# Optimization experiments

Measured on AMD Instinct MI355X. Metric: run time of the kernel, lower is better.

## Reference

```python
import jax, jax.numpy as jnp
import numpy as np

T, B, E, H, F = 1024, 2, 1024, 16, 8
D = E // H
R = 2 * T - 1  # relative positions T-1 .. -(T-1)


def setup_inputs() -> dict:
    key = jax.random.key(0)
    ks = jax.random.split(key, 11)
    std = float(np.sqrt(2.0 / (E + E)))
    return {
        "input": jax.random.normal(ks[0], (T, B, E), jnp.float32),
        "pos": jax.random.normal(ks[1], (R, B, E), jnp.float32),
        "factor": jax.random.normal(ks[2], (F,), jnp.float32),
        "in_proj_weight": jax.random.normal(ks[3], (3 * E * E, F), jnp.float32) * std,
        "pos_proj_weight": jax.random.normal(ks[4], (E * E, F), jnp.float32) * std,
        "out_proj_weight": jax.random.normal(ks[5], (E * E, F), jnp.float32) * std,
        "in_proj_bias": jax.random.normal(ks[6], (3 * E, F), jnp.float32) * 0.02,
        "pos_proj_bias": jax.random.normal(ks[7], (E, F), jnp.float32) * 0.02,
        "out_proj_bias": jax.random.normal(ks[8], (E, F), jnp.float32) * 0.02,
        "r_w_bias": jax.random.normal(ks[9], (E, F), jnp.float32) * 0.02,
        "r_r_bias": jax.random.normal(ks[10], (E, F), jnp.float32) * 0.02,
    }


def _rel_shift(x):
    # x: [BH, T, R] -> out[b, i, j] = x[b, i, j + (T-1) - i]
    bh, q, r = x.shape
    zp = jnp.zeros((bh, q, 1), x.dtype)
    xp = jnp.concatenate([zp, x], axis=2).reshape(bh, r + 1, q)
    return xp[:, 1:, :].reshape(bh, q, r)


def reference(input, pos, factor, in_proj_weight, pos_proj_weight, out_proj_weight,
              in_proj_bias, pos_proj_bias, out_proj_bias, r_w_bias, r_r_bias):
    # hypernetwork: generate effective weights from factor vector (torch.mv)
    W_in = (in_proj_weight @ factor).reshape(3 * E, E)
    W_pos = (pos_proj_weight @ factor).reshape(E, E)
    W_out = (out_proj_weight @ factor).reshape(E, E)
    b_in = in_proj_bias @ factor
    b_pos = pos_proj_bias @ factor
    b_out = out_proj_bias @ factor
    rw = (r_w_bias @ factor).reshape(H, D)  # content bias
    rr = (r_r_bias @ factor).reshape(H, D)  # position bias

    qkv = input @ W_in.T + b_in                      # [T, B, 3E]
    q, k, v = jnp.split(qkv, 3, axis=-1)
    q = q.reshape(T, B, H, D)
    k = k.reshape(T, B, H, D)
    v = v.reshape(T, B, H, D)
    r = (pos @ W_pos.T + b_pos).reshape(R, B, H, D)  # [R, B, H, D]

    scale = 1.0 / np.sqrt(D)
    # AC: content-content + content bias term
    AC = jnp.einsum('ibhd,jbhd->bhij', q + rw, k)    # [B, H, T, T]
    # BD: content-position + position bias term, then relative shift
    BD = jnp.einsum('ibhd,rbhd->bhir', q + rr, r)    # [B, H, T, R]
    BD = _rel_shift(BD.reshape(B * H, T, R))[:, :, :T].reshape(B, H, T, T)

    attn = jax.nn.softmax((AC + BD) * scale, axis=-1)  # [B, H, T, T]
    out = jnp.einsum('bhij,jbhd->ibhd', attn, v).reshape(T, B, E)
    out = out @ W_out.T + b_out                       # [T, B, E]
    return out
```

## Files before the change

### kernel.cpp

```cpp
#include <hip/hip_runtime.h>


typedef _Float16 h16;
typedef _Float16 h16x8 __attribute__((ext_vector_type(8)));
typedef _Float16 h16x4 __attribute__((ext_vector_type(4)));
typedef float f32x4 __attribute__((ext_vector_type(4)));

static __device__ __forceinline__ f32x4 mfma16(h16x8 a, h16x8 b, f32x4 c) {
  return __builtin_amdgcn_mfma_f32_16x16x32_f16(a, b, c, 0, 0, 0);
}
static __device__ __forceinline__ void gload16(const void* g, void* l) {
  __builtin_amdgcn_global_load_lds((const __attribute__((address_space(1))) void*)g,
                                   (__attribute__((address_space(3))) void*)l, 16, 0, 0);
}

__global__ __launch_bounds__(256) void hypernet_kernel(
    const float* __restrict__ fac,
    const float* __restrict__ w_in, const float* __restrict__ w_pos,
    const float* __restrict__ w_out, const float* __restrict__ b_in_w,
    const float* __restrict__ b_pos_w, const float* __restrict__ b_out_w,
    const float* __restrict__ rw_w, const float* __restrict__ rr_w,
    h16* __restrict__ Win, h16* __restrict__ Wpos, h16* __restrict__ Wout,
    float* __restrict__ bin, float* __restrict__ bpos, float* __restrict__ bout,
    float* __restrict__ rw, float* __restrict__ rr, h16* __restrict__ rb,
    const float* __restrict__ input, h16* __restrict__ in_h,
    const float* __restrict__ pos, h16* __restrict__ pos_h)
{
  int idx = blockIdx.x * 256 + threadIdx.x;
  float f0=fac[0],f1=fac[1],f2=fac[2],f3=fac[3],f4=fac[4],f5=fac[5],f6=fac[6],f7=fac[7];
#define DOT8(p) ((p)[0]*f0+(p)[1]*f1+(p)[2]*f2+(p)[3]*f3+(p)[4]*f4+(p)[5]*f5+(p)[6]*f6+(p)[7]*f7)
  if (idx < 3145728) { const float* p = w_in  + (size_t)idx*8; Win[idx]  = (h16)DOT8(p); return; }
  idx -= 3145728;
  if (idx < 1048576) { const float* p = w_pos + (size_t)idx*8; Wpos[idx] = (h16)DOT8(p); return; }
  idx -= 1048576;
  if (idx < 1048576) { const float* p = w_out + (size_t)idx*8; Wout[idx] = (h16)DOT8(p); return; }
  idx -= 1048576;
  if (idx < 3072) { bin[idx]  = DOT8(b_in_w  + (size_t)idx*8); return; }
  idx -= 3072;
  if (idx < 1024) { bpos[idx] = DOT8(b_pos_w + (size_t)idx*8); return; }
  idx -= 1024;
  if (idx < 1024) { bout[idx] = DOT8(b_out_w + (size_t)idx*8); return; }
  idx -= 1024;
  if (idx < 1024) { rw[idx]   = DOT8(rw_w    + (size_t)idx*8); return; }
  idx -= 1024;
  if (idx < 1024) { rr[idx]   = DOT8(rr_w    + (size_t)idx*8); return; }
  idx -= 1024;
  if (idx < 2048) { rb[(((size_t)(idx >> 6)) << 17) + 2047*64 + (idx & 63)] = (h16)0.f; return; }
  idx -= 2048;
  if (idx < 524288) {
    float4 v = reinterpret_cast<const float4*>(input)[idx];
    h16x4 o = { (h16)v.x, (h16)v.y, (h16)v.z, (h16)v.w };
    reinterpret_cast<h16x4*>(in_h)[idx] = o;
    return;
  }
  idx -= 524288;
  if (idx < 1048064) {
    float4 v = reinterpret_cast<const float4*>(pos)[idx];
    h16x4 o = { (h16)v.x, (h16)v.y, (h16)v.z, (h16)v.w };
    reinterpret_cast<h16x4*>(pos_h)[idx] = o;
  }
#undef DOT8
}

template <int MODE>
__global__ __launch_bounds__(256) void gemm_lds_kernel(
    const h16* __restrict__ A, const h16* __restrict__ Bw,
    const float* __restrict__ bias, int M, int N, int K,
    float* __restrict__ Cout,
    const float* __restrict__ rwv, const float* __restrict__ rrv,
    h16* __restrict__ o0, h16* __restrict__ o1,
    h16* __restrict__ o2, h16* __restrict__ o3)
{
  __shared__ __align__(16) h16 a_sm[128*64];
  __shared__ __align__(16) h16 b_sm[128*64];
  const int tid = threadIdx.x, lane = tid & 63, wave = tid >> 6;
  const int quad = lane >> 4, t16 = lane & 15;
  const int wm = wave >> 1, wn = wave & 1;
  const int m0 = blockIdx.y * 128, n0 = blockIdx.x * 128;
  const int lrow = lane >> 3, lgran = lane & 7;
  const int gsw = (lgran ^ lrow) * 8;
  const int xg0 = (quad ^ (t16 & 7)) * 8;
  const int xg1 = xg0 ^ 32;

  f32x4 acc[4][4];
#pragma unroll
  for (int i = 0; i < 4; ++i)
#pragma unroll
    for (int j = 0; j < 4; ++j) acc[i][j] = (f32x4){0.f,0.f,0.f,0.f};

  for (int k0 = 0; k0 < K; k0 += 64) {
    __syncthreads();
#pragma unroll
    for (int s = 0; s < 4; ++s) {
      int rbase = wave*32 + s*8;
      gload16(A  + (size_t)(m0 + rbase + lrow)*K + k0 + gsw, a_sm + rbase*64);
      gload16(Bw + (size_t)(n0 + rbase + lrow)*K + k0 + gsw, b_sm + rbase*64);
    }
    __syncthreads();
#pragma unroll
    for (int kc = 0; kc < 2; ++kc) {
      const int xg = kc ? xg1 : xg0;
      h16x8 af[4], bfr[4];
#pragma unroll
      for (int i = 0; i < 4; ++i) {
        af[i]  = *reinterpret_cast<const h16x8*>(a_sm + (wm*64 + i*16 + t16)*64 + xg);
        bfr[i] = *reinterpret_cast<const h16x8*>(b_sm + (wn*64 + i*16 + t16)*64 + xg);
      }
#pragma unroll
      for (int i = 0; i < 4; ++i)
#pragma unroll
        for (int j = 0; j < 4; ++j)
          acc[i][j] = mfma16(af[i], bfr[j], acc[i][j]);
    }
  }

#pragma unroll
  for (int i = 0; i < 4; ++i) {
    int mb = m0 + wm*64 + i*16 + quad*4;
#pragma unroll
    for (int j = 0; j < 4; ++j) {
      int n = n0 + wn*64 + j*16 + t16;
      float bv = bias[n];
      if (MODE == 2) {
#pragma unroll
        for (int r = 0; r < 4; ++r)
          Cout[(size_t)(mb + r)*N + n] = acc[i][j][r] + bv;
      } else if (MODE == 0) {
        int nn = n & 1023, sec = n >> 10, hh = nn >> 6, d = nn & 63;
        float rwb = rwv[nn], rrb = rrv[nn];
#pragma unroll
        for (int r = 0; r < 4; ++r) {
          int m = mb + r, t = m >> 1, b = m & 1;
          size_t off = ((size_t)((b << 4) + hh) << 16) + (t << 6) + d;
          float v = acc[i][j][r] + bv;
          if (sec == 0)      { o0[off] = (h16)(v + rwb); o1[off] = (h16)(v + rrb); }
          else if (sec == 1) { o2[off] = (h16)v; }
          else               { o3[off] = (h16)v; }
        }
      } else {
        int hh = n >> 6, d = n & 63;
#pragma unroll
        for (int r = 0; r < 4; ++r) {
          int m = mb + r;
          if (m < M) {
            int rel = m >> 1, b = m & 1;
            o0[(((size_t)((b << 4) + hh)) << 17) + (rel << 6) + d] = (h16)(acc[i][j][r] + bv);
          }
        }
      }
    }
  }
}

__global__ __launch_bounds__(256) void transpose_v_kernel(
    const h16* __restrict__ vb, h16* __restrict__ vbt)
{
  __shared__ h16 tile[64*72];
  const int bh = blockIdx.y, t0 = blockIdx.x * 64;
  const int r = threadIdx.x >> 3, c = (threadIdx.x & 7) * 8;
  const h16* src = vb + ((size_t)bh << 16) + (size_t)(t0 + r)*64 + c;
  *reinterpret_cast<h16x8*>(tile + r*72 + c)        = *reinterpret_cast<const h16x8*>(src);
  *reinterpret_cast<h16x8*>(tile + (r + 32)*72 + c) = *reinterpret_cast<const h16x8*>(src + 32*64);
  __syncthreads();
  h16x8 o0, o1;
#pragma unroll
  for (int e = 0; e < 8; ++e) {
    o0[e] = tile[(c + e)*72 + r];
    o1[e] = tile[(c + e)*72 + r + 32];
  }
  h16* dst = vbt + ((size_t)bh << 16) + (size_t)r*1024 + t0 + c;
  *reinterpret_cast<h16x8*>(dst)            = o0;
  *reinterpret_cast<h16x8*>(dst + 32*1024)  = o1;
}

__global__ __launch_bounds__(256) void flash_kernel(
    const h16* __restrict__ qrw, const h16* __restrict__ qrr,
    const h16* __restrict__ kb, const h16* __restrict__ vbt,
    const h16* __restrict__ rb,
    float* __restrict__ o_part, float* __restrict__ ml_part)
{
  __shared__ __align__(16) h16 k_sm[64*64];
  __shared__ __align__(16) h16 vt_sm[64*64];
  __shared__ __align__(16) h16 r_sm[128*64];

  const int tid = threadIdx.x, lane = tid & 63, wave = tid >> 6;
  const int quad = lane >> 4, t16 = lane & 15;
  const int bh = blockIdx.y, i0 = blockIdx.x * 64, jh = blockIdx.z;
  const size_t base  = (size_t)bh << 16;
  const size_t rbase = (size_t)bh << 17;
  const int iw = i0 + wave * 16;
  const int lrow = lane >> 3, lgran = lane & 7;
  const int gsw = (lgran ^ lrow) * 8;
  const int xg0 = (quad ^ (t16 & 7)) * 8;
  const int xg1 = xg0 ^ 32;

  h16x8 a_rw[2], a_rr[2];
  {
    const h16* p = qrw + base + (size_t)(iw + t16)*64 + quad*8;
    a_rw[0] = *reinterpret_cast<const h16x8*>(p);
    a_rw[1] = *reinterpret_cast<const h16x8*>(p + 32);
    const h16* p2 = qrr + base + (size_t)(iw + t16)*64 + quad*8;
    a_rr[0] = *reinterpret_cast<const h16x8*>(p2);
    a_rr[1] = *reinterpret_cast<const h16x8*>(p2 + 32);
  }

  f32x4 o_acc[4];
#pragma unroll
  for (int dc = 0; dc < 4; ++dc) o_acc[dc] = (f32x4){0.f,0.f,0.f,0.f};
  float m_run[4] = {-1e30f,-1e30f,-1e30f,-1e30f};
  float l_run[4] = {0.f,0.f,0.f,0.f};

  h16* bdw = r_sm + wave * (16*84);
  const int cb0 = 3 - wave;

  for (int j0 = jh*256; j0 < jh*256 + 256; j0 += 64) {
    __syncthreads();
    {
#pragma unroll
      for (int s = 0; s < 2; ++s) {
        int row = wave*16 + s*8;
        gload16(kb  + base + (size_t)(j0 + row + lrow)*64 + gsw, k_sm  + row*64);
        gload16(vbt + base + (size_t)(row + lrow)*1024 + j0 + gsw, vt_sm + row*64);
      }
      const int rel0 = j0 - i0 + 960;
#pragma unroll
      for (int s = 0; s < 4; ++s) {
        int row = wave*32 + s*8;
        gload16(rb + rbase + (size_t)(rel0 + row + lrow)*64 + gsw, r_sm + row*64);
      }
    }
    __syncthreads();

    f32x4 s_ac[4];
#pragma unroll
    for (int c = 0; c < 4; ++c) {
      s_ac[c] = (f32x4){0.f,0.f,0.f,0.f};
      s_ac[c] = mfma16(a_rw[0], *reinterpret_cast<const h16x8*>(k_sm + (c*16 + t16)*64 + xg0), s_ac[c]);
      s_ac[c] = mfma16(a_rw[1], *reinterpret_cast<const h16x8*>(k_sm + (c*16 + t16)*64 + xg1), s_ac[c]);
    }
    f32x4 s_bd[5];
#pragma unroll
    for (int u = 0; u < 5; ++u) {
      s_bd[u] = (f32x4){0.f,0.f,0.f,0.f};
      s_bd[u] = mfma16(a_rr[0], *reinterpret_cast<const h16x8*>(r_sm + ((cb0+u)*16 + t16)*64 + xg0), s_bd[u]);
      s_bd[u] = mfma16(a_rr[1], *reinterpret_cast<const h16x8*>(r_sm + ((cb0+u)*16 + t16)*64 + xg1), s_bd[u]);
    }
    __syncthreads();

#pragma unroll
    for (int u = 0; u < 5; ++u)
#pragma unroll
      for (int r = 0; r < 4; ++r)
        bdw[(quad*4 + r)*84 + u*16 + t16] = (h16)s_bd[u][r];

    float sv[4][4];
#pragma unroll
    for (int c = 0; c < 4; ++c)
#pragma unroll
      for (int r = 0; r < 4; ++r) {
        int il = quad*4 + r;
        float bdv = (float)bdw[il*84 + c*16 + t16 + 15 - il];
        sv[c][r] = (s_ac[c][r] + bdv) * 0.125f;
      }

    float alpha[4];
#pragma unroll
    for (int r = 0; r < 4; ++r) {
      float v = fmaxf(fmaxf(sv[0][r], sv[1][r]), fmaxf(sv[2][r], sv[3][r]));
#pragma unroll
      for (int off = 1; off < 16; off <<= 1) v = fmaxf(v, __shfl_xor(v, off, 64));
      float mn = fmaxf(m_run[r], v);
      alpha[r] = __expf(m_run[r] - mn);
      m_run[r] = mn;
    }
#pragma unroll
    for (int r = 0; r < 4; ++r) {
      float s0 = 0.f;
#pragma unroll
      for (int c = 0; c < 4; ++c) {
        float p = __expf(sv[c][r] - m_run[r]);
        sv[c][r] = p; s0 += p;
      }
      l_run[r] = l_run[r]*alpha[r] + s0;
    }
#pragma unroll
    for (int dc = 0; dc < 4; ++dc) {
      f32x4 t = o_acc[dc];
#pragma unroll
      for (int r = 0; r < 4; ++r) t[r] *= alpha[r];
      o_acc[dc] = t;
    }
    h16* pw = bdw;
#pragma unroll
    for (int c = 0; c < 4; ++c)
#pragma unroll
      for (int r = 0; r < 4; ++r)
        pw[(quad*4 + r)*72 + c*16 + t16] = (h16)sv[c][r];

    h16x8 ap0 = *reinterpret_cast<const h16x8*>(pw + t16*72 + quad*8);
    h16x8 ap1 = *reinterpret_cast<const h16x8*>(pw + t16*72 + 32 + quad*8);
#pragma unroll
    for (int dc = 0; dc < 4; ++dc) {
      h16x8 bv0 = *reinterpret_cast<const h16x8*>(vt_sm + (dc*16 + t16)*64 + xg0);
      h16x8 bv1 = *reinterpret_cast<const h16x8*>(vt_sm + (dc*16 + t16)*64 + xg1);
      o_acc[dc] = mfma16(ap0, bv0, o_acc[dc]);
      o_acc[dc] = mfma16(ap1, bv1, o_acc[dc]);
    }
  }

#pragma unroll
  for (int r = 0; r < 4; ++r) {
    float l = l_run[r];
#pragma unroll
    for (int off = 1; off < 16; off <<= 1) l += __shfl_xor(l, off, 64);
    l_run[r] = l;
  }
  const size_t obase = ((size_t)jh*32 + bh) * 1024 * 64;
#pragma unroll
  for (int r = 0; r < 4; ++r) {
    int i = iw + quad*4 + r;
#pragma unroll
    for (int dc = 0; dc < 4; ++dc)
      o_part[obase + (size_t)i*64 + dc*16 + t16] = o_acc[dc][r];
    if (t16 == 0) {
      size_t mo = (((size_t)jh*32 + bh)*1024 + i)*2;
      ml_part[mo]     = m_run[r];
      ml_part[mo + 1] = l_run[r];
    }
  }
}

__global__ __launch_bounds__(256) void combine_kernel(
    const float* __restrict__ o_part, const float* __restrict__ ml_part,
    h16* __restrict__ attn_h)
{
  int gid = blockIdx.x * 256 + threadIdx.x;
  int row = gid >> 4;
  int d4 = (gid & 15) * 4;
  float m[4], l[4];
#pragma unroll
  for (int p = 0; p < 4; ++p) {
    m[p] = ml_part[p*65536 + row*2];
    l[p] = ml_part[p*65536 + row*2 + 1];
  }
  float M = fmaxf(fmaxf(m[0], m[1]), fmaxf(m[2], m[3]));
  float e[4], den = 0.f;
#pragma unroll
  for (int p = 0; p < 4; ++p) { e[p] = __expf(m[p] - M); den += e[p]*l[p]; }
  float inv = 1.f / den;
  float4 acc = {0.f,0.f,0.f,0.f};
#pragma unroll
  for (int p = 0; p < 4; ++p) {
    float4 O = *reinterpret_cast<const float4*>(o_part + (size_t)p*2097152 + (size_t)row*64 + d4);
    acc.x += e[p]*O.x; acc.y += e[p]*O.y; acc.z += e[p]*O.z; acc.w += e[p]*O.w;
  }
  int bh = row >> 10, i = row & 1023, b = bh >> 4, h = bh & 15;
  h16x4 o = { (h16)(acc.x*inv), (h16)(acc.y*inv), (h16)(acc.z*inv), (h16)(acc.w*inv) };
  *reinterpret_cast<h16x4*>(attn_h + ((size_t)(i*2 + b))*1024 + h*64 + d4) = o;
}

extern "C" void kernel_launch(void* const* d_in, const int* in_sizes, int n_in,
                              void* d_out, int out_size, void* d_ws, size_t ws_size,
                              hipStream_t stream)
{
  const float* input  = (const float*)d_in[0];
  const float* pos    = (const float*)d_in[1];
  const float* fac    = (const float*)d_in[2];
  const float* w_in   = (const float*)d_in[3];
  const float* w_pos  = (const float*)d_in[4];
  const float* w_out  = (const float*)d_in[5];
  const float* bin_w  = (const float*)d_in[6];
  const float* bpos_w = (const float*)d_in[7];
  const float* bout_w = (const float*)d_in[8];
  const float* rw_w   = (const float*)d_in[9];
  const float* rr_w   = (const float*)d_in[10];
  float* out = (float*)d_out;
  (void)in_sizes; (void)n_in; (void)out_size; (void)ws_size;

  char* w = (char*)d_ws;
  auto take = [&](size_t bytes) { char* p = w; w += bytes; return p; };
  h16*   Win    = (h16*)take(3145728ull*2);
  h16*   Wpos   = (h16*)take(1048576ull*2);
  h16*   Wout   = (h16*)take(1048576ull*2);
  float* bin    = (float*)take(3072*4);
  float* bpos   = (float*)take(1024*4);
  float* bout   = (float*)take(1024*4);
  float* rw     = (float*)take(1024*4);
  float* rr     = (float*)take(1024*4);
  h16*   in_h   = (h16*)take(2097152ull*2);
  h16*   pos_h  = (h16*)take(4192256ull*2);
  h16*   qrwb   = (h16*)take(2097152ull*2);
  h16*   qrrb   = (h16*)take(2097152ull*2);
  h16*   kb     = (h16*)take(2097152ull*2);
  h16*   vb     = (h16*)take(2097152ull*2);
  h16*   vbt    = (h16*)take(2097152ull*2);
  h16*   rb     = (h16*)take(4194304ull*2);
  float* o_part = (float*)take(4ull*2097152ull*4);
  float* ml     = (float*)take(4ull*65536ull*4);
  h16*   attn_h = (h16*)take(2097152ull*2);

  hypernet_kernel<<<26658, 256, 0, stream>>>(fac, w_in, w_pos, w_out, bin_w, bpos_w, bout_w,
                                             rw_w, rr_w, Win, Wpos, Wout, bin, bpos, bout,
                                             rw, rr, rb, input, in_h, pos, pos_h);
  gemm_lds_kernel<0><<<dim3(24, 16), 256, 0, stream>>>(in_h, Win, bin, 2048, 3072, 1024,
                                                       nullptr, rw, rr, qrwb, qrrb, kb, vb);
  gemm_lds_kernel<1><<<dim3(8, 32), 256, 0, stream>>>(pos_h, Wpos, bpos, 4094, 1024, 1024,
                                                      nullptr, nullptr, nullptr, rb, nullptr, nullptr, nullptr);
  transpose_v_kernel<<<dim3(16, 32), 256, 0, stream>>>(vb, vbt);
  flash_kernel<<<dim3(16, 32, 4), 256, 0, stream>>>(qrwb, qrrb, kb, vbt, rb, o_part, ml);
  combine_kernel<<<2048, 256, 0, stream>>>(o_part, ml, attn_h);
  gemm_lds_kernel<2><<<dim3(8, 16), 256, 0, stream>>>(attn_h, Wout, bout, 2048, 1024, 1024,
                                                      out, nullptr, nullptr, nullptr, nullptr, nullptr, nullptr);
}
```

Measured before the change: 356.7 us.

## Vectorize hypernet weight generation and fuse V transpose into QKV GEMM epilogue

The hypernetwork kernel now handles eight outputs per thread. It uses float4 loads of each 8-wide factor row and writes into the contiguous Win/Wpos/Wout and in_h/pos_h workspace regions as single flat arrays, which cuts the grid size and per-thread branching. The separate V transpose kernel and its intermediate buffer are removed. The QKV GEMM epilogue now writes V directly in transposed [d, t] layout. This saves a launch and a round trip through memory, but the new scattered 2-byte epilogue stores have a 1024-element stride and are poorly coalesced.

```diff
diff --git a/kernel.cpp b/kernel.cpp
--- a/kernel.cpp
+++ b/kernel.cpp
@@ -20,46 +20,83 @@
     const float* __restrict__ w_out, const float* __restrict__ b_in_w,
     const float* __restrict__ b_pos_w, const float* __restrict__ b_out_w,
     const float* __restrict__ rw_w, const float* __restrict__ rr_w,
-    h16* __restrict__ Win, h16* __restrict__ Wpos, h16* __restrict__ Wout,
+    h16* __restrict__ Wall,
     float* __restrict__ bin, float* __restrict__ bpos, float* __restrict__ bout,
     float* __restrict__ rw, float* __restrict__ rr, h16* __restrict__ rb,
-    const float* __restrict__ input, h16* __restrict__ in_h,
-    const float* __restrict__ pos, h16* __restrict__ pos_h)
+    const float* __restrict__ input, const float* __restrict__ pos,
+    h16* __restrict__ cast_h)
 {
-  int idx = blockIdx.x * 256 + threadIdx.x;
-  float f0=fac[0],f1=fac[1],f2=fac[2],f3=fac[3],f4=fac[4],f5=fac[5],f6=fac[6],f7=fac[7];
-#define DOT8(p) ((p)[0]*f0+(p)[1]*f1+(p)[2]*f2+(p)[3]*f3+(p)[4]*f4+(p)[5]*f5+(p)[6]*f6+(p)[7]*f7)
-  if (idx < 3145728) { const float* p = w_in  + (size_t)idx*8; Win[idx]  = (h16)DOT8(p); return; }
-  idx -= 3145728;
-  if (idx < 1048576) { const float* p = w_pos + (size_t)idx*8; Wpos[idx] = (h16)DOT8(p); return; }
-  idx -= 1048576;
-  if (idx < 1048576) { const float* p = w_out + (size_t)idx*8; Wout[idx] = (h16)DOT8(p); return; }
-  idx -= 1048576;
-  if (idx < 3072) { bin[idx]  = DOT8(b_in_w  + (size_t)idx*8); return; }
-  idx -= 3072;
-  if (idx < 1024) { bpos[idx] = DOT8(b_pos_w + (size_t)idx*8); return; }
-  idx -= 1024;
-  if (idx < 1024) { bout[idx] = DOT8(b_out_w + (size_t)idx*8); return; }
-  idx -= 1024;
-  if (idx < 1024) { rw[idx]   = DOT8(rw_w    + (size_t)idx*8); return; }
-  idx -= 1024;
-  if (idx < 1024) { rr[idx]   = DOT8(rr_w    + (size_t)idx*8); return; }
-  idx -= 1024;
-  if (idx < 2048) { rb[(((size_t)(idx >> 6)) << 17) + 2047*64 + (idx & 63)] = (h16)0.f; return; }
-  idx -= 2048;
-  if (idx < 524288) {
-    float4 v = reinterpret_cast<const float4*>(input)[idx];
-    h16x4 o = { (h16)v.x, (h16)v.y, (h16)v.z, (h16)v.w };
-    reinterpret_cast<h16x4*>(in_h)[idx] = o;
+  const int tid = threadIdx.x;
+  const float f0=fac[0],f1=fac[1],f2=fac[2],f3=fac[3],
+              f4=fac[4],f5=fac[5],f6=fac[6],f7=fac[7];
+#define DOT(a,b) ((a).x*f0+(a).y*f1+(a).z*f2+(a).w*f3+(b).x*f4+(b).y*f5+(b).z*f6+(b).w*f7)
+
+  if (blockIdx.x < 2560) {
+    const int base = blockIdx.x * 2048 + tid;
+    float4 va[8], vb[8];
+#pragma unroll
+    for (int k = 0; k < 8; ++k) {
+      int r = base + k*256;
+      const float4* s;
+      if (r < 3145728)      s = reinterpret_cast<const float4*>(w_in  + (size_t)r*8);
+      else if (r < 4194304) s = reinterpret_cast<const float4*>(w_pos + (size_t)(r-3145728)*8);
+      else                  s = reinterpret_cast<const float4*>(w_out + (size_t)(r-4194304)*8);
+      va[k] = s[0]; vb[k] = s[1];
+    }
+#pragma unroll
+    for (int k = 0; k < 8; ++k)
+      Wall[base + k*256] = (h16)DOT(va[k], vb[k]);
     return;
   }
-  idx -= 524288;
-  if (idx < 1048064) {
-    float4 v = reinterpret_cast<const float4*>(pos)[idx];
-    h16x4 o = { (h16)v.x, (h16)v.y, (h16)v.z, (h16)v.w };
-    reinterpret_cast<h16x4*>(pos_h)[idx] = o;
-  }
-#undef DOT8
+  if (blockIdx.x < 2596) {
+    int idx = (blockIdx.x - 2560) * 256 + tid;
+    if (idx < 3072) {
+      const float4* s = reinterpret_cast<const float4*>(b_in_w + (size_t)idx*8);
+      bin[idx] = DOT(s[0], s[1]); return;
+    }
+    idx -= 3072;
+    if (idx < 1024) {
+      const float4* s = reinterpret_cast<const float4*>(b_pos_w + (size_t)idx*8);
+      bpos[idx] = DOT(s[0], s[1]); return;
+    }
+    idx -= 1024;
+    if (idx < 1024) {
+      const float4* s = reinterpret_cast<const float4*>(b_out_w + (size_t)idx*8);
+      bout[idx] = DOT(s[0], s[1]); return;
+    }
+    idx -= 1024;
+    if (idx < 1024) {
+      const float4* s = reinterpret_cast<const float4*>(rw_w + (size_t)idx*8);
+      rw[idx] = DOT(s[0], s[1]); return;
+    }
+    idx -= 1024;
+    if (idx < 1024) {
+      const float4* s = reinterpret_cast<const float4*>(rr_w + (size_t)idx*8);
+      rr[idx] = DOT(s[0], s[1]); return;
+    }
+    idx -= 1024;
+    if (idx < 2048)
+      rb[(((size_t)(idx >> 6)) << 17) + 2047*64 + (idx & 63)] = (h16)0.f;
+    return;
+  }
+  {
+    const int base = (blockIdx.x - 2596) * 2048 + tid;
+    float4 v[8]; int g[8];
+#pragma unroll
+    for (int k = 0; k < 8; ++k) {
+      g[k] = base + k*256;
+      if (g[k] < 1572352)
+        v[k] = (g[k] < 524288) ? reinterpret_cast<const float4*>(input)[g[k]]
+                               : reinterpret_cast<const float4*>(pos)[g[k] - 524288];
+    }
+#pragma unroll
+    for (int k = 0; k < 8; ++k)
+      if (g[k] < 1572352) {
+        h16x4 o = { (h16)v[k].x, (h16)v[k].y, (h16)v[k].z, (h16)v[k].w };
+        reinterpret_cast<h16x4*>(cast_h)[g[k]] = o;
+      }
+  }
+#undef DOT
 }
 
 template <int MODE>
@@ -131,11 +168,12 @@
 #pragma unroll
         for (int r = 0; r < 4; ++r) {
           int m = mb + r, t = m >> 1, b = m & 1;
-          size_t off = ((size_t)((b << 4) + hh) << 16) + (t << 6) + d;
+          size_t hbase = (size_t)((b << 4) + hh) << 16;
           float v = acc[i][j][r] + bv;
-          if (sec == 0)      { o0[off] = (h16)(v + rwb); o1[off] = (h16)(v + rrb); }
-          else if (sec == 1) { o2[off] = (h16)v; }
-          else               { o3[off] = (h16)v; }
+          if (sec == 0)      { o0[hbase + (t << 6) + d] = (h16)(v + rwb);
+                               o1[hbase + (t << 6) + d] = (h16)(v + rrb); }
+          else if (sec == 1) { o2[hbase + (t << 6) + d] = (h16)v; }
+          else               { o3[hbase + (d << 10) + t] = (h16)v; }
         }
       } else {
         int hh = n >> 6, d = n & 63;
@@ -150,27 +188,6 @@
       }
     }
   }
-}
-
-__global__ __launch_bounds__(256) void transpose_v_kernel(
-    const h16* __restrict__ vb, h16* __restrict__ vbt)
-{
-  __shared__ h16 tile[64*72];
-  const int bh = blockIdx.y, t0 = blockIdx.x * 64;
-  const int r = threadIdx.x >> 3, c = (threadIdx.x & 7) * 8;
-  const h16* src = vb + ((size_t)bh << 16) + (size_t)(t0 + r)*64 + c;
-  *reinterpret_cast<h16x8*>(tile + r*72 + c)        = *reinterpret_cast<const h16x8*>(src);
-  *reinterpret_cast<h16x8*>(tile + (r + 32)*72 + c) = *reinterpret_cast<const h16x8*>(src + 32*64);
-  __syncthreads();
-  h16x8 o0, o1;
-#pragma unroll
-  for (int e = 0; e < 8; ++e) {
-    o0[e] = tile[(c + e)*72 + r];
-    o1[e] = tile[(c + e)*72 + r + 32];
-  }
-  h16* dst = vbt + ((size_t)bh << 16) + (size_t)r*1024 + t0 + c;
-  *reinterpret_cast<h16x8*>(dst)            = o0;
-  *reinterpret_cast<h16x8*>(dst + 32*1024)  = o1;
 }
 
 __global__ __launch_bounds__(256) void flash_kernel(
@@ -392,21 +409,19 @@
   h16*   qrwb   = (h16*)take(2097152ull*2);
   h16*   qrrb   = (h16*)take(2097152ull*2);
   h16*   kb     = (h16*)take(2097152ull*2);
-  h16*   vb     = (h16*)take(2097152ull*2);
   h16*   vbt    = (h16*)take(2097152ull*2);
   h16*   rb     = (h16*)take(4194304ull*2);
   float* o_part = (float*)take(4ull*2097152ull*4);
   float* ml     = (float*)take(4ull*65536ull*4);
   h16*   attn_h = (h16*)take(2097152ull*2);
 
-  hypernet_kernel<<<26658, 256, 0, stream>>>(fac, w_in, w_pos, w_out, bin_w, bpos_w, bout_w,
-                                             rw_w, rr_w, Win, Wpos, Wout, bin, bpos, bout,
-                                             rw, rr, rb, input, in_h, pos, pos_h);
+  hypernet_kernel<<<3364, 256, 0, stream>>>(fac, w_in, w_pos, w_out, bin_w, bpos_w, bout_w,
+                                            rw_w, rr_w, Win, bin, bpos, bout,
+                                            rw, rr, rb, input, pos, in_h);
   gemm_lds_kernel<0><<<dim3(24, 16), 256, 0, stream>>>(in_h, Win, bin, 2048, 3072, 1024,
-                                                       nullptr, rw, rr, qrwb, qrrb, kb, vb);
+                                                       nullptr, rw, rr, qrwb, qrrb, kb, vbt);
   gemm_lds_kernel<1><<<dim3(8, 32), 256, 0, stream>>>(pos_h, Wpos, bpos, 4094, 1024, 1024,
                                                       nullptr, nullptr, nullptr, rb, nullptr, nullptr, nullptr);
-  transpose_v_kernel<<<dim3(16, 32), 256, 0, stream>>>(vb, vbt);
   flash_kernel<<<dim3(16, 32, 4), 256, 0, stream>>>(qrwb, qrrb, kb, vbt, rb, o_part, ml);
   combine_kernel<<<2048, 256, 0, stream>>>(o_part, ml, attn_h);
   gemm_lds_kernel<2><<<dim3(8, 16), 256, 0, stream>>>(attn_h, Wout, bout, 2048, 1024, 1024,
```

After: 371.1 us. +4.0%, slower.
